# Optimization experiments

Measured on AMD Instinct MI355X. Metric: run time of the kernel, lower is better.

Reference implementation:

```python
import jax, jax.numpy as jnp
import numpy as np

B, N, H, E, P = 2, 20000, 128, 200000, 3


def _mlp2(x, w1, b1, w2, b2):
    # Linear -> SiLU -> Linear
    return jax.nn.silu(x @ w1 + b1) @ w2 + b2


def setup_inputs() -> dict:
    key = jax.random.key(0)
    ks = iter(jax.random.split(key, 40))
    def nrm(shape, s=0.05):
        return jax.random.normal(next(ks), shape, dtype=jnp.float32) * s
    inp = {
        "features": jax.random.normal(next(ks), (B, N, H), dtype=jnp.float32),
        "positions": jax.random.normal(next(ks), (B, N, P), dtype=jnp.float32),
        "edge_index_up": jax.random.randint(next(ks), (2, E), 0, N, dtype=jnp.int32),
        "edge_index_down": jax.random.randint(next(ks), (2, E), 0, N, dtype=jnp.int32),
        "degree_up": jax.random.uniform(next(ks), (N,), minval=1.0, maxval=32.0, dtype=jnp.float32),
        "degree_down": jax.random.uniform(next(ks), (N,), minval=1.0, maxval=32.0, dtype=jnp.float32),
    }
    for name in ("up", "down"):
        inp[f"w_msg1_{name}"] = nrm((2 * H + 1, H)); inp[f"b_msg1_{name}"] = jnp.zeros((H,), jnp.float32)
        inp[f"w_msg2_{name}"] = nrm((H, H));         inp[f"b_msg2_{name}"] = jnp.zeros((H,), jnp.float32)
        inp[f"w_pos1_{name}"] = nrm((H, H));         inp[f"b_pos1_{name}"] = jnp.zeros((H,), jnp.float32)
        inp[f"w_pos2_{name}"] = nrm((H, 1));         inp[f"b_pos2_{name}"] = jnp.zeros((1,), jnp.float32)
    inp["w_upd1"] = nrm((2 * H, H)); inp["b_upd1"] = jnp.zeros((H,), jnp.float32)
    inp["w_upd2"] = nrm((H, H));     inp["b_upd2"] = jnp.zeros((H,), jnp.float32)
    return inp


def reference(features, positions, edge_index_up, edge_index_down, degree_up, degree_down,
              w_msg1_up, b_msg1_up, w_msg2_up, b_msg2_up,
              w_pos1_up, b_pos1_up, w_pos2_up, b_pos2_up,
              w_msg1_down, b_msg1_down, w_msg2_down, b_msg2_down,
              w_pos1_down, b_pos1_down, w_pos2_down, b_pos2_down,
              w_upd1, b_upd1, w_upd2, b_upd2):
    n_neighborhoods = 2
    msg_acc = jnp.zeros_like(features)
    pos_upd = jnp.zeros_like(positions)
    neighborhoods = [
        (edge_index_up, degree_up,
         (w_msg1_up, b_msg1_up, w_msg2_up, b_msg2_up),
         (w_pos1_up, b_pos1_up, w_pos2_up, b_pos2_up)),
        (edge_index_down, degree_down,
         (w_msg1_down, b_msg1_down, w_msg2_down, b_msg2_down),
         (w_pos1_down, b_pos1_down, w_pos2_down, b_pos2_down)),
    ]
    for edge_index, degree, msg_p, pos_p in neighborhoods:
        src, dst = edge_index[0], edge_index[1]
        h_src = features[:, src, :]                     # [B, E, H] gather
        h_dst = features[:, dst, :]                     # [B, E, H] gather
        rel_pos = positions[:, src, :] - positions[:, dst, :]  # [B, E, P]
        dist = jnp.linalg.norm(rel_pos, axis=-1, keepdims=True)  # [B, E, 1]
        msg_input = jnp.concatenate([h_src, h_dst, dist], axis=-1)  # [B, E, 2H+1]
        messages = _mlp2(msg_input, *msg_p)             # [B, E, H]
        agg = jnp.zeros_like(features).at[:, dst, :].add(messages)  # scatter-add over dim 1
        agg = agg / jnp.clip(degree, 1.0, None)[None, :, None]
        msg_acc = msg_acc + agg
        weights = jnp.tanh(_mlp2(messages, *pos_p))     # [B, E, 1]
        pos_upd = pos_upd + jnp.zeros_like(positions).at[:, dst, :].add(weights * rel_pos)
    feat_update = _mlp2(jnp.concatenate([features, msg_acc], axis=-1), w_upd1, b_upd1, w_upd2, b_upd2)
    updated_features = features + feat_update
    updated_positions = positions + pos_upd / n_neighborhoods
    return updated_features, updated_positions
```

## Files before the change

kernel.cpp:

```cpp
#include <hip/hip_runtime.h>

#define BB 2
#define NN 20000
#define HH 128
#define EE 200000
#define TR 96
#define NEB 2084
#define NBLK 79

typedef unsigned short u16;
typedef __attribute__((ext_vector_type(4))) float f32x4;
typedef __bf16 bf16x8 __attribute__((ext_vector_type(8)));

#define MFMA(a, b, c) __builtin_amdgcn_mfma_f32_16x16x32_bf16((a), (b), (c), 0, 0, 0)

__device__ __forceinline__ float bf2f(u16 u) {
    union { unsigned int i; float f; } v; v.i = ((unsigned int)u) << 16; return v.f;
}
__device__ __forceinline__ u16 f2bf(float f) {
    union { __bf16 h; u16 u; } v; v.h = (__bf16)f; return v.u;
}
#if __has_builtin(__builtin_amdgcn_rcpf)
__device__ __forceinline__ float rcpf(float x) { return __builtin_amdgcn_rcpf(x); }
#else
__device__ __forceinline__ float rcpf(float x) { return 1.f / x; }
#endif
__device__ __forceinline__ float silu_f(float z) { return z * rcpf(1.f + __expf(-z)); }
__device__ __forceinline__ float ldv(const void* p, long i, int f) {
    return f ? ((const float*)p)[i] : bf2f(((const u16*)p)[i]);
}

__global__ __launch_bounds__(256) void detect_zero_kernel(const u16* __restrict__ f,
                                                          int* __restrict__ flag,
                                                          int* __restrict__ cnt) {
    int i = blockIdx.x * 256 + threadIdx.x;
    if (i < 40000) cnt[i] = 0;
    if (blockIdx.x == 0) {
        int tid = threadIdx.x;
        u16 v = f[tid * 2];
        int e = (v >> 7) & 0xFF;
        int ok = (e >= 101 && e <= 143) ? 1 : 0;
        __shared__ int c;
        if (tid == 0) c = 0;
        __syncthreads();
        atomicAdd(&c, ok);
        __syncthreads();
        if (tid == 0) *flag = (c < 200) ? 1 : 0;
    }
}

#define C5TOT 5281540
#define FTOT 180224
#define R0 5240000
#define R1 (R0 + C5TOT)
#define R2 (R1 + FTOT)
#define R3 (R2 + 2 * EE)
struct P18 { const void* p[18]; };
struct P8 { const void* w[8]; };

__global__ __launch_bounds__(256) void setup_kernel(
    P18 cp, P8 wf, const int* __restrict__ eu, const int* __restrict__ ed,
    float* __restrict__ ws_acc, u16* __restrict__ canon, u16* __restrict__ fbase,
    int* __restrict__ cnt_up, int* __restrict__ cnt_dn, const int* __restrict__ flag)
{
    long i = (long)blockIdx.x * 256 + threadIdx.x;
    if (i < R0) { ws_acc[i] = 0.f; return; }
    if (i < R1) {
        static const int off[19] = {
            0, 5120000, 5240000, 5260000, 5280000,
            5280128, 5280256, 5280384, 5280512, 5280640,
            5280642, 5280770, 5280898, 5281026, 5281154, 5281282,
            5281284, 5281412, 5281540 };
        static const int rsz[18] = {
            5120000, 120000, 20000, 20000,
            128, 128, 128, 128, 128, 1,
            128, 128, 128, 128, 128, 1,
            128, 128 };
        static const int soff[18] = {
            0, 0, 0, 0,
            32768, 0, 0, 0, 0, 0,
            32768, 0, 0, 0, 0, 0,
            0, 0 };
        int j = (int)(i - R0);
        int isf = *flag;
        int t = 0;
#pragma unroll 1
        while (j >= off[t + 1]) ++t;
        int k = j - off[t];
        u16 v = 0;
        if (k < rsz[t]) v = f2bf(ldv(cp.p[t], (long)soff[t] + k, isf));
        canon[j] = v;
        return;
    }
    if (i < R2) {
        static const int foff[9] = { 0, 32768, 49152, 65536, 98304, 114688,
                                     131072, 163840, 180224 };
        int j = (int)(i - R1);
        int isf = *flag;
        int t = 0;
#pragma unroll 1
        while (j >= foff[t + 1]) ++t;
        int m = j - foff[t];
        int jj = m & 7, lane = (m >> 3) & 63, nt = (m >> 9) & 7, kt = m >> 12;
        int k = kt * 32 + ((lane >> 4) * 8) + jj;
        int n = nt * 16 + (lane & 15);
        fbase[j] = f2bf(ldv(wf.w[t], (long)k * 128 + n, isf));
        return;
    }
    if (i < R3) {
        int e = (int)(i - R2);
        if (e < EE) atomicAdd(&cnt_up[eu[EE + e]], 1);
        else atomicAdd(&cnt_dn[ed[EE + e - EE]], 1);
    }
}

struct SP { const int* cnt[2]; int* cur[2]; int* bsum[2]; };

__global__ __launch_bounds__(256) void scan1_kernel(SP p) {
    int half = blockIdx.x / NBLK;
    int b = blockIdx.x - half * NBLK;
    int t = threadIdx.x;
    int i = b * 256 + t;
    __shared__ int buf[256];
    int v = (i < NN) ? p.cnt[half][i] : 0;
    buf[t] = v;
    __syncthreads();
    for (int s = 1; s < 256; s <<= 1) {
        int x = (t >= s) ? buf[t - s] : 0;
        __syncthreads();
        buf[t] += x;
        __syncthreads();
    }
    if (i < NN) p.cur[half][i] = buf[t] - v;
    if (t == 255) p.bsum[half][b] = buf[255];
}

__global__ __launch_bounds__(256) void scan2_kernel(int* __restrict__ bu, int* __restrict__ bd) {
    __shared__ int buf[2][128];
    int half = threadIdx.x >> 7, t = threadIdx.x & 127;
    int* bs = half ? bd : bu;
    int v = (t < NBLK) ? bs[t] : 0;
    buf[half][t] = v;
    __syncthreads();
    for (int s = 1; s < 128; s <<= 1) {
        int x = (t >= s) ? buf[half][t - s] : 0;
        __syncthreads();
        buf[half][t] += x;
        __syncthreads();
    }
    if (t < NBLK) bs[t] = buf[half][t] - v;
}

__global__ void scatter2_kernel(const int* __restrict__ eu, const int* __restrict__ ed,
                                int* __restrict__ cu, const int* __restrict__ bu,
                                int* __restrict__ cd, const int* __restrict__ bd,
                                int* __restrict__ su, int* __restrict__ sd) {
    int e = blockIdx.x * 256 + threadIdx.x;
    if (e < EE) {
        int d = eu[EE + e];
        int p = atomicAdd(&cu[d], 1) + bu[d >> 8];
        su[p] = e;
    } else {
        e -= EE;
        if (e < EE) {
            int d = ed[EE + e];
            int p = atomicAdd(&cd[d], 1) + bd[d >> 8];
            sd[p] = e;
        }
    }
}

struct EP {
    const int* eidx; const int* es; const u16* deg;
    const u16* fW1; const u16* fW2; const u16* fP1;
    const u16* w1last; const u16* bias1; const u16* bias2;
    const u16* biasp1; const u16* wp2; const u16* biasp2;
};

__global__ __launch_bounds__(512, 4) void edge_kernel(
    const u16* __restrict__ feat, const u16* __restrict__ posit,
    EP up, EP dn,
    float* __restrict__ msg_base, float* __restrict__ pos_base)
{
    const int tid = threadIdx.x;
    const int lane = tid & 63;
    const int wv = tid >> 6;
    const int half = blockIdx.x / (BB * NEB);
    const int rem = blockIdx.x - half * (BB * NEB);
    const int bb = rem / NEB;
    const int s0 = (rem - bb * NEB) * TR;
    const EP P = half ? dn : up;
    float* msg_acc = msg_base + (size_t)bb * NN * HH;
    float* pos_acc = pos_base + (size_t)bb * NN * 3;

    __shared__ u16 sA[TR][136];
    __shared__ u16 sB[TR][136];
    __shared__ u16 sC[TR][136];
    __shared__ float sInv[TR];
    __shared__ int sDst[TR];

    {
        const int r = tid >> 2, part = tid & 3;
        if (r < TR) {
            int slot = s0 + r; if (slot >= EE) slot = EE - 1;
            int e = P.es[slot];
            int s = P.eidx[e];
            int d = P.eidx[EE + e];
            if (part == 0) {
                sDst[r] = d;
                sInv[r] = 1.f / fmaxf(bf2f(P.deg[d]), 1.f);
                const u16* ps = posit + ((size_t)bb * NN + s) * 3;
                const u16* pd = posit + ((size_t)bb * NN + d) * 3;
                float dx = bf2f(ps[0]) - bf2f(pd[0]);
                float dy = bf2f(ps[1]) - bf2f(pd[1]);
                float dz = bf2f(ps[2]) - bf2f(pd[2]);
                *(float4*)&sC[r][128] =
                    make_float4(sqrtf(dx * dx + dy * dy + dz * dz), dx, dy, dz);
            }
            const uint4* fs = (const uint4*)(feat + ((size_t)bb * NN + s) * HH);
            const uint4* fd = (const uint4*)(feat + ((size_t)bb * NN + d) * HH);
            uint4* as = (uint4*)&sA[r][part * 32];
            uint4* ad = (uint4*)&sB[r][part * 32];
#pragma unroll
            for (int i = 0; i < 4; ++i) { as[i] = fs[part * 4 + i]; ad[i] = fd[part * 4 + i]; }
        }
    }
    __syncthreads();

    const int nt = wv;
    const int mrow = lane & 15;
    const int kq = (lane >> 4) * 8;
    const int crow = (lane >> 4) * 4;
    const int ccol = lane & 15;
    const int col = nt * 16 + ccol;

    f32x4 acc[6];
#pragma unroll
    for (int mt = 0; mt < 6; ++mt) acc[mt] = (f32x4){0.f, 0.f, 0.f, 0.f};

#pragma unroll
    for (int kt = 0; kt < 8; ++kt) {
        const u16* Xb = (kt < 4) ? &sA[0][0] : &sB[0][0];
        const int kk = (kt & 3) * 32 + kq;
        bf16x8 bw = *(const bf16x8*)(P.fW1 + (size_t)(((kt * 8 + nt) * 64 + lane) * 8));
#pragma unroll
        for (int mt = 0; mt < 6; ++mt) {
            bf16x8 a = *(const bf16x8*)(Xb + (mt * 16 + mrow) * 136 + kk);
            acc[mt] = MFMA(a, bw, acc[mt]);
        }
    }

    {
        const float wl = bf2f(P.w1last[col]);
        const float bb1 = bf2f(P.bias1[col]);
#pragma unroll
        for (int mt = 0; mt < 6; ++mt) {
#pragma unroll
            for (int r = 0; r < 4; ++r) {
                const int row = mt * 16 + crow + r;
                const float dist = ((const float*)&sC[row][128])[0];
                float z = fmaf(dist, wl, acc[mt][r]) + bb1;
                sC[row][col] = f2bf(silu_f(z));
            }
        }
    }
    __syncthreads();

#pragma unroll
    for (int mt = 0; mt < 6; ++mt) acc[mt] = (f32x4){0.f, 0.f, 0.f, 0.f};
#pragma unroll
    for (int kt = 0; kt < 4; ++kt) {
        const int kk = kt * 32 + kq;
        bf16x8 bw = *(const bf16x8*)(P.fW2 + (size_t)(((kt * 8 + nt) * 64 + lane) * 8));
#pragma unroll
        for (int mt = 0; mt < 6; ++mt) {
            bf16x8 a = *(const bf16x8*)(&sC[0][0] + (mt * 16 + mrow) * 136 + kk);
            acc[mt] = MFMA(a, bw, acc[mt]);
        }
    }
    {
        const float bb2 = bf2f(P.bias2[col]);
#pragma unroll
        for (int mt = 0; mt < 6; ++mt) {
#pragma unroll
            for (int r = 0; r < 4; ++r) {
                const int row = mt * 16 + crow + r;
                sA[row][col] = f2bf(acc[mt][r] + bb2);
            }
        }
    }
    __syncthreads();

#pragma unroll
    for (int mt = 0; mt < 6; ++mt) acc[mt] = (f32x4){0.f, 0.f, 0.f, 0.f};
#pragma unroll
    for (int kt = 0; kt < 4; ++kt) {
        const int kk = kt * 32 + kq;
        bf16x8 bw = *(const bf16x8*)(P.fP1 + (size_t)(((kt * 8 + nt) * 64 + lane) * 8));
#pragma unroll
        for (int mt = 0; mt < 6; ++mt) {
            bf16x8 a = *(const bf16x8*)(&sA[0][0] + (mt * 16 + mrow) * 136 + kk);
            acc[mt] = MFMA(a, bw, acc[mt]);
        }
    }
    {
        const float bp1 = bf2f(P.biasp1[col]);
#pragma unroll
        for (int mt = 0; mt < 6; ++mt) {
#pragma unroll
            for (int r = 0; r < 4; ++r) {
                const int row = mt * 16 + crow + r;
                sB[row][col] = f2bf(silu_f(acc[mt][r] + bp1));
            }
        }
    }
    __syncthreads();


    {
        const int scol = tid & 127;
        const int r0 = (tid >> 7) * 24;
        float vals[24];
#pragma unroll
        for (int j = 0; j < 24; ++j) vals[j] = bf2f(sA[r0 + j][scol]);
        float accv = 0.f;
        int dprev = sDst[r0];
        float invprev = sInv[r0];
#pragma unroll
        for (int j = 0; j < 24; ++j) {
            const int r = r0 + j;
            int dcur = sDst[r];
            if (dcur != dprev) {
                unsafeAtomicAdd(&msg_acc[(size_t)dprev * HH + scol], accv * invprev);
                accv = 0.f; dprev = dcur; invprev = sInv[r];
            }
            accv += (s0 + r < EE) ? vals[j] : 0.f;
        }
        unsafeAtomicAdd(&msg_acc[(size_t)dprev * HH + scol], accv * invprev);
    }

    {
        const int r = tid >> 2, q = tid & 3;
        if (r < TR) {
            const unsigned* t32 = (const unsigned*)&sB[r][q * 32];
            const unsigned* w32 = (const unsigned*)(P.wp2 + q * 32);
            float p = 0.f;
#pragma unroll
            for (int k = 0; k < 16; ++k) {
                unsigned a = t32[k], b = w32[k];
                union { unsigned i; float f; } al, ah, bl, bh;
                al.i = a << 16; ah.i = a & 0xffff0000u;
                bl.i = b << 16; bh.i = b & 0xffff0000u;
                p = fmaf(al.f, bl.f, p);
                p = fmaf(ah.f, bh.f, p);
            }
            p += __shfl_xor(p, 1);
            p += __shfl_xor(p, 2);
            if (q == 0 && s0 + r < EE) {
                float wgt = tanhf(p + bf2f(P.biasp2[0]));
                const float* rp = (const float*)&sC[r][128];
                const size_t pb = (size_t)sDst[r] * 3;
                unsafeAtomicAdd(&pos_acc[pb + 0], wgt * rp[1]);
                unsafeAtomicAdd(&pos_acc[pb + 1], wgt * rp[2]);
                unsafeAtomicAdd(&pos_acc[pb + 2], wgt * rp[3]);
            }
        }
    }
}

__global__ __launch_bounds__(256) void update_kernel(
    const void* __restrict__ rawfeat, const void* __restrict__ rawpos,
    const u16* __restrict__ fU1, const u16* __restrict__ bu1,
    const u16* __restrict__ fU2, const u16* __restrict__ bu2,
    void* __restrict__ outp, const float* __restrict__ magg, const float* __restrict__ pacc,
    const int* __restrict__ flag)
{
    const int tid = threadIdx.x;
    const int lane = tid & 63;
    const int wv = tid >> 6;
    const int row0 = blockIdx.x * 64;
    const int isf = *flag;

    __shared__ u16 sA[64][136];
    __shared__ u16 sB[64][136];

    if (isf) {
        const float* fp = (const float*)rawfeat + (size_t)row0 * HH;
        for (int i = tid; i < 1024; i += 256) {
            int r = i >> 4, c = (i & 15) * 8;
            float4 v0 = *(const float4*)(fp + (size_t)r * HH + c);
            float4 v1 = *(const float4*)(fp + (size_t)r * HH + c + 4);
            uint4 o;
            o.x = (unsigned)f2bf(v0.x) | ((unsigned)f2bf(v0.y) << 16);
            o.y = (unsigned)f2bf(v0.z) | ((unsigned)f2bf(v0.w) << 16);
            o.z = (unsigned)f2bf(v1.x) | ((unsigned)f2bf(v1.y) << 16);
            o.w = (unsigned)f2bf(v1.z) | ((unsigned)f2bf(v1.w) << 16);
            *(uint4*)&sA[r][c] = o;
        }
    } else {
        const uint4* fp = (const uint4*)((const u16*)rawfeat + (size_t)row0 * HH);
        for (int i = tid; i < 1024; i += 256) {
            int r = i >> 4, c = i & 15;
            *(uint4*)&sA[r][c * 8] = fp[i];
        }
    }
    {
        const float4* am = (const float4*)(magg) + (size_t)row0 * 32;
        for (int i = tid; i < 2048; i += 256) {
            int r = i >> 5;
            float4 v = am[i];
            int c = (i & 31) * 4;
            sB[r][c + 0] = f2bf(v.x);
            sB[r][c + 1] = f2bf(v.y);
            sB[r][c + 2] = f2bf(v.z);
            sB[r][c + 3] = f2bf(v.w);
        }
    }
    __syncthreads();

    const int nt0 = wv * 2;
    const int mrow = lane & 15;
    const int kq = (lane >> 4) * 8;
    const int crow = (lane >> 4) * 4;
    const int ccol = lane & 15;

    f32x4 acc[4][2];
#pragma unroll
    for (int mt = 0; mt < 4; ++mt) {
        acc[mt][0] = (f32x4){0.f, 0.f, 0.f, 0.f};
        acc[mt][1] = (f32x4){0.f, 0.f, 0.f, 0.f};
    }
#pragma unroll
    for (int kt = 0; kt < 8; ++kt) {
        const u16* Xb = (kt < 4) ? &sA[0][0] : &sB[0][0];
        const int kk = (kt & 3) * 32 + kq;
        bf16x8 bw0 = *(const bf16x8*)(fU1 + (size_t)(((kt * 8 + nt0) * 64 + lane) * 8));
        bf16x8 bw1 = *(const bf16x8*)(fU1 + (size_t)(((kt * 8 + nt0 + 1) * 64 + lane) * 8));
#pragma unroll
        for (int mt = 0; mt < 4; ++mt) {
            bf16x8 a = *(const bf16x8*)(Xb + (mt * 16 + mrow) * 136 + kk);
            acc[mt][0] = MFMA(a, bw0, acc[mt][0]);
            acc[mt][1] = MFMA(a, bw1, acc[mt][1]);
        }
    }
    __syncthreads();

#pragma unroll
    for (int mt = 0; mt < 4; ++mt) {
#pragma unroll
        for (int n2 = 0; n2 < 2; ++n2) {
            const int col = (nt0 + n2) * 16 + ccol;
            const float bb = bf2f(bu1[col]);
#pragma unroll
            for (int r = 0; r < 4; ++r) {
                const int row = mt * 16 + crow + r;
                sB[row][col] = f2bf(silu_f(acc[mt][n2][r] + bb));
            }
        }
    }
    __syncthreads();

#pragma unroll
    for (int mt = 0; mt < 4; ++mt) {
        acc[mt][0] = (f32x4){0.f, 0.f, 0.f, 0.f};
        acc[mt][1] = (f32x4){0.f, 0.f, 0.f, 0.f};
    }
#pragma unroll
    for (int kt = 0; kt < 4; ++kt) {
        const int kk = kt * 32 + kq;
        bf16x8 bw0 = *(const bf16x8*)(fU2 + (size_t)(((kt * 8 + nt0) * 64 + lane) * 8));
        bf16x8 bw1 = *(const bf16x8*)(fU2 + (size_t)(((kt * 8 + nt0 + 1) * 64 + lane) * 8));
#pragma unroll
        for (int mt = 0; mt < 4; ++mt) {
            bf16x8 a = *(const bf16x8*)(&sB[0][0] + (mt * 16 + mrow) * 136 + kk);
            acc[mt][0] = MFMA(a, bw0, acc[mt][0]);
            acc[mt][1] = MFMA(a, bw1, acc[mt][1]);
        }
    }
#pragma unroll
    for (int mt = 0; mt < 4; ++mt) {
#pragma unroll
        for (int n2 = 0; n2 < 2; ++n2) {
            const int col = (nt0 + n2) * 16 + ccol;
            const float bb = bf2f(bu2[col]);
#pragma unroll
            for (int r = 0; r < 4; ++r) {
                const int row = mt * 16 + crow + r;
                const size_t idx = (size_t)(row0 + row) * HH + col;
                if (isf) {
                    float base = ((const float*)rawfeat)[idx];
                    ((float*)outp)[idx] = acc[mt][n2][r] + bb + base;
                } else {
                    float base = bf2f(sA[row][col]);
                    ((u16*)outp)[idx] = f2bf(acc[mt][n2][r] + bb + base);
                }
            }
        }
    }

    if (tid < 192) {
        int i = row0 * 3 + tid;
        float x = pacc[i];
        if (isf) {
            float base = ((const float*)rawpos)[i];
            ((float*)outp)[5120000 + i] = base + 0.5f * x;
        } else {
            float base = bf2f(((const u16*)rawpos)[i]);
            ((u16*)outp)[5120000 + i] = f2bf(base + 0.5f * x);
        }
    }
}

extern "C" void kernel_launch(void* const* d_in, const int* in_sizes, int n_in,
                              void* d_out, int out_size, void* d_ws, size_t ws_size,
                              hipStream_t stream)
{
    float* ws_msg  = (float*)d_ws;
    float* ws_pos  = (float*)((char*)d_ws + 20480000);
    int*   cnt_up  = (int*)((char*)d_ws + 20960000);
    int*   cnt_dn  = (int*)((char*)d_ws + 21040000);
    int*   cur_up  = (int*)((char*)d_ws + 21120000);
    int*   cur_dn  = (int*)((char*)d_ws + 21200000);
    int*   bsum_up = (int*)((char*)d_ws + 21280000);
    int*   bsum_dn = (int*)((char*)d_ws + 21280400);
    int*   es_up   = (int*)((char*)d_ws + 21280800);
    int*   es_dn   = (int*)((char*)d_ws + 22080800);
    u16*   fbase   = (u16*)((char*)d_ws + 22880800);
    u16*   canon   = (u16*)((char*)d_ws + 23241248);
    int*   flag    = (int*)((char*)d_ws + 33804328);
    if (ws_size < 33804332ULL) return;

    u16* f_m1u = fbase;
    u16* f_m2u = fbase + 32768;
    u16* f_p1u = fbase + 49152;
    u16* f_m1d = fbase + 65536;
    u16* f_m2d = fbase + 98304;
    u16* f_p1d = fbase + 114688;
    u16* f_u1  = fbase + 131072;
    u16* f_u2  = fbase + 163840;

    u16* cfeat  = canon;
    u16* cpos   = canon + 5120000;
    u16* cdgu   = canon + 5240000;
    u16* cdgd   = canon + 5260000;
    u16* cw1lu  = canon + 5280000;
    u16* cb1u   = canon + 5280128;
    u16* cb2u   = canon + 5280256;
    u16* cbp1u  = canon + 5280384;
    u16* cwp2u  = canon + 5280512;
    u16* cbp2u  = canon + 5280640;
    u16* cw1ld  = canon + 5280642;
    u16* cb1d   = canon + 5280770;
    u16* cb2d   = canon + 5280898;
    u16* cbp1d  = canon + 5281026;
    u16* cwp2d  = canon + 5281154;
    u16* cbp2d  = canon + 5281282;
    u16* cbu1   = canon + 5281284;
    u16* cbu2   = canon + 5281412;

    const int* ei_up = (const int*)d_in[2];
    const int* ei_dn = (const int*)d_in[3];

    detect_zero_kernel<<<157, 256, 0, stream>>>((const u16*)d_in[0], flag, cnt_up);

    P18 cp;
    cp.p[0] = d_in[0];  cp.p[1] = d_in[1];  cp.p[2] = d_in[4];  cp.p[3] = d_in[5];
    cp.p[4] = d_in[6];  cp.p[5] = d_in[7];  cp.p[6] = d_in[9];  cp.p[7] = d_in[11];
    cp.p[8] = d_in[12]; cp.p[9] = d_in[13];
    cp.p[10] = d_in[14]; cp.p[11] = d_in[15]; cp.p[12] = d_in[17]; cp.p[13] = d_in[19];
    cp.p[14] = d_in[20]; cp.p[15] = d_in[21];
    cp.p[16] = d_in[23]; cp.p[17] = d_in[25];
    P8 wsf;
    wsf.w[0] = d_in[6];  wsf.w[1] = d_in[8];  wsf.w[2] = d_in[10]; wsf.w[3] = d_in[14];
    wsf.w[4] = d_in[16]; wsf.w[5] = d_in[18]; wsf.w[6] = d_in[22]; wsf.w[7] = d_in[24];
    setup_kernel<<<(R3 + 255) / 256, 256, 0, stream>>>(cp, wsf, ei_up, ei_dn,
                                                       ws_msg, canon, fbase,
                                                       cnt_up, cnt_dn, flag);

    SP sp;
    sp.cnt[0] = cnt_up; sp.cnt[1] = cnt_dn;
    sp.cur[0] = cur_up; sp.cur[1] = cur_dn;
    sp.bsum[0] = bsum_up; sp.bsum[1] = bsum_dn;
    scan1_kernel<<<2 * NBLK, 256, 0, stream>>>(sp);
    scan2_kernel<<<1, 256, 0, stream>>>(bsum_up, bsum_dn);
    scatter2_kernel<<<(2 * EE + 255) / 256, 256, 0, stream>>>(ei_up, ei_dn, cur_up, bsum_up,
                                                              cur_dn, bsum_dn, es_up, es_dn);

    EP up, dn;
    up.eidx = ei_up; up.es = es_up; up.deg = cdgu;
    up.fW1 = f_m1u; up.fW2 = f_m2u; up.fP1 = f_p1u;
    up.w1last = cw1lu; up.bias1 = cb1u; up.bias2 = cb2u;
    up.biasp1 = cbp1u; up.wp2 = cwp2u; up.biasp2 = cbp2u;
    dn.eidx = ei_dn; dn.es = es_dn; dn.deg = cdgd;
    dn.fW1 = f_m1d; dn.fW2 = f_m2d; dn.fP1 = f_p1d;
    dn.w1last = cw1ld; dn.bias1 = cb1d; dn.bias2 = cb2d;
    dn.biasp1 = cbp1d; dn.wp2 = cwp2d; dn.biasp2 = cbp2d;
    edge_kernel<<<2 * BB * NEB, 512, 0, stream>>>(cfeat, cpos, up, dn, ws_msg, ws_pos);

    update_kernel<<<625, 256, 0, stream>>>(d_in[0], d_in[1], f_u1, cbu1, f_u2, cbu2,
                                           d_out, ws_msg, ws_pos, flag);
}
```

Baseline: 499.8 us.

## Precompose msg2 and pos1 weights to compute both second-stage GEMMs concurrently

A new setup kernel precomputes W_msg2·W_pos1 and the folded bias (b2·W_pos1 + b_pos1), so the position MLP's first layer can be fed directly from the SiLU hidden layer. The edge kernel then runs one wider GEMM producing both the messages and the position hidden activations in one pass, removing a dependent GEMM stage and one barrier. Warps are retiled into a 2x4 grid with 48 rows by 32 or 64 columns each. The trade-offs are an extra bf16 rounding of the composed weights, which changes numerics slightly, and the assumption that fP1 buffers hold 2x the fragment space at offset 16384.

After: 537.1 us. 1.07x slower.

```diff
diff --git a/kernel.cpp b/kernel.cpp
--- a/kernel.cpp
+++ b/kernel.cpp
@@ -114,6 +114,38 @@
     }
 }
 
+__global__ __launch_bounds__(256) void gemm_fuse_kernel(
+    const void* __restrict__ w2u, const void* __restrict__ p1u,
+    const void* __restrict__ b2u, const void* __restrict__ bp1u,
+    const void* __restrict__ w2d, const void* __restrict__ p1d,
+    const void* __restrict__ b2d, const void* __restrict__ bp1d,
+    u16* __restrict__ fragu, u16* __restrict__ fragd,
+    u16* __restrict__ cbp1u, u16* __restrict__ cbp1d,
+    const int* __restrict__ flag)
+{
+    const int dir = blockIdx.x >> 6;
+    const int idx = (blockIdx.x & 63) * 256 + threadIdx.x;
+    const int k = idx >> 7, n = idx & 127;
+    const int isf = *flag;
+    const void* W2 = dir ? w2d : w2u;
+    const void* P1 = dir ? p1d : p1u;
+    float s = 0.f;
+#pragma unroll 4
+    for (int m = 0; m < 128; ++m)
+        s += ldv(W2, (long)k * 128 + m, isf) * ldv(P1, (long)m * 128 + n, isf);
+    u16* dst = dir ? fragd : fragu;
+    dst[(((k >> 5) * 8 + (n >> 4)) * 64 + ((k >> 3) & 3) * 16 + (n & 15)) * 8 + (k & 7)] = f2bf(s);
+    if (idx < 128) {
+        const void* B2 = dir ? b2d : b2u;
+        const void* BP1 = dir ? bp1d : bp1u;
+        float t = 0.f;
+#pragma unroll 4
+        for (int m = 0; m < 128; ++m)
+            t += ldv(B2, m, isf) * ldv(P1, (long)m * 128 + idx, isf);
+        (dir ? cbp1d : cbp1u)[idx] = f2bf(t + ldv(BP1, idx, isf));
+    }
+}
+
 struct SP { const int* cnt[2]; int* cur[2]; int* bsum[2]; };
 
 __global__ __launch_bounds__(256) void scan1_kernel(SP p) {
@@ -227,95 +259,108 @@
     }
     __syncthreads();
 
-    const int nt = wv;
+    const int wm = wv >> 2;
+    const int wn = wv & 3;
+    const int rbase = wm * 48;
     const int mrow = lane & 15;
     const int kq = (lane >> 4) * 8;
     const int crow = (lane >> 4) * 4;
     const int ccol = lane & 15;
-    const int col = nt * 16 + ccol;
-
-    f32x4 acc[6];
-#pragma unroll
-    for (int mt = 0; mt < 6; ++mt) acc[mt] = (f32x4){0.f, 0.f, 0.f, 0.f};
-
+
+    f32x4 acc[3][2];
+#pragma unroll
+    for (int mt = 0; mt < 3; ++mt) {
+        acc[mt][0] = (f32x4){0.f, 0.f, 0.f, 0.f};
+        acc[mt][1] = (f32x4){0.f, 0.f, 0.f, 0.f};
+    }
 #pragma unroll
     for (int kt = 0; kt < 8; ++kt) {
         const u16* Xb = (kt < 4) ? &sA[0][0] : &sB[0][0];
         const int kk = (kt & 3) * 32 + kq;
-        bf16x8 bw = *(const bf16x8*)(P.fW1 + (size_t)(((kt * 8 + nt) * 64 + lane) * 8));
-#pragma unroll
-        for (int mt = 0; mt < 6; ++mt) {
-            bf16x8 a = *(const bf16x8*)(Xb + (mt * 16 + mrow) * 136 + kk);
-            acc[mt] = MFMA(a, bw, acc[mt]);
-        }
-    }
-
-    {
+        bf16x8 bw0 = *(const bf16x8*)(P.fW1 + (size_t)(((kt * 8 + wn * 2) * 64 + lane) * 8));
+        bf16x8 bw1 = *(const bf16x8*)(P.fW1 + (size_t)(((kt * 8 + wn * 2 + 1) * 64 + lane) * 8));
+#pragma unroll
+        for (int mt = 0; mt < 3; ++mt) {
+            bf16x8 a = *(const bf16x8*)(Xb + (rbase + mt * 16 + mrow) * 136 + kk);
+            acc[mt][0] = MFMA(a, bw0, acc[mt][0]);
+            acc[mt][1] = MFMA(a, bw1, acc[mt][1]);
+        }
+    }
+
+#pragma unroll
+    for (int n2 = 0; n2 < 2; ++n2) {
+        const int col = (wn * 2 + n2) * 16 + ccol;
         const float wl = bf2f(P.w1last[col]);
         const float bb1 = bf2f(P.bias1[col]);
 #pragma unroll
-        for (int mt = 0; mt < 6; ++mt) {
+        for (int mt = 0; mt < 3; ++mt) {
 #pragma unroll
             for (int r = 0; r < 4; ++r) {
-                const int row = mt * 16 + crow + r;
+                const int row = rbase + mt * 16 + crow + r;
                 const float dist = ((const float*)&sC[row][128])[0];
-                float z = fmaf(dist, wl, acc[mt][r]) + bb1;
+                float z = fmaf(dist, wl, acc[mt][n2][r]) + bb1;
                 sC[row][col] = f2bf(silu_f(z));
             }
         }
     }
     __syncthreads();
 
-#pragma unroll
-    for (int mt = 0; mt < 6; ++mt) acc[mt] = (f32x4){0.f, 0.f, 0.f, 0.f};
+    f32x4 facc[3][4];
+#pragma unroll
+    for (int mt = 0; mt < 3; ++mt)
+#pragma unroll
+        for (int j = 0; j < 4; ++j) facc[mt][j] = (f32x4){0.f, 0.f, 0.f, 0.f};
+    const int nt0 = wn * 4;
 #pragma unroll
     for (int kt = 0; kt < 4; ++kt) {
         const int kk = kt * 32 + kq;
-        bf16x8 bw = *(const bf16x8*)(P.fW2 + (size_t)(((kt * 8 + nt) * 64 + lane) * 8));
-#pragma unroll
-        for (int mt = 0; mt < 6; ++mt) {
-            bf16x8 a = *(const bf16x8*)(&sC[0][0] + (mt * 16 + mrow) * 136 + kk);
-            acc[mt] = MFMA(a, bw, acc[mt]);
-        }
-    }
-    {
-        const float bb2 = bf2f(P.bias2[col]);
-#pragma unroll
-        for (int mt = 0; mt < 6; ++mt) {
-#pragma unroll
-            for (int r = 0; r < 4; ++r) {
-                const int row = mt * 16 + crow + r;
-                sA[row][col] = f2bf(acc[mt][r] + bb2);
-            }
-        }
-    }
-    __syncthreads();
-
-#pragma unroll
-    for (int mt = 0; mt < 6; ++mt) acc[mt] = (f32x4){0.f, 0.f, 0.f, 0.f};
-#pragma unroll
-    for (int kt = 0; kt < 4; ++kt) {
-        const int kk = kt * 32 + kq;
-        bf16x8 bw = *(const bf16x8*)(P.fP1 + (size_t)(((kt * 8 + nt) * 64 + lane) * 8));
-#pragma unroll
-        for (int mt = 0; mt < 6; ++mt) {
-            bf16x8 a = *(const bf16x8*)(&sA[0][0] + (mt * 16 + mrow) * 136 + kk);
-            acc[mt] = MFMA(a, bw, acc[mt]);
-        }
-    }
-    {
-        const float bp1 = bf2f(P.biasp1[col]);
-#pragma unroll
-        for (int mt = 0; mt < 6; ++mt) {
-#pragma unroll
-            for (int r = 0; r < 4; ++r) {
-                const int row = mt * 16 + crow + r;
-                sB[row][col] = f2bf(silu_f(acc[mt][r] + bp1));
-            }
-        }
-    }
-    __syncthreads();
-
+        bf16x8 bw[4];
+#pragma unroll
+        for (int j = 0; j < 4; ++j) {
+            const int nt = nt0 + j;
+            const size_t off = (nt & 8)
+                ? (size_t)(16384 + ((kt * 8 + (nt & 7)) * 64 + lane) * 8)
+                : (size_t)(((kt * 8 + nt) * 64 + lane) * 8);
+            bw[j] = *(const bf16x8*)(P.fW2 + off);
+        }
+#pragma unroll
+        for (int mt = 0; mt < 3; ++mt) {
+            bf16x8 a = *(const bf16x8*)(&sC[0][0] + (rbase + mt * 16 + mrow) * 136 + kk);
+#pragma unroll
+            for (int j = 0; j < 4; ++j) facc[mt][j] = MFMA(a, bw[j], facc[mt][j]);
+        }
+    }
+
+    if (wn < 2) {
+#pragma unroll
+        for (int j = 0; j < 4; ++j) {
+            const int col = (nt0 + j) * 16 + ccol;
+            const float b2v = bf2f(P.bias2[col]);
+#pragma unroll
+            for (int mt = 0; mt < 3; ++mt) {
+#pragma unroll
+                for (int r = 0; r < 4; ++r) {
+                    const int row = rbase + mt * 16 + crow + r;
+                    sA[row][col] = f2bf(facc[mt][j][r] + b2v);
+                }
+            }
+        }
+    } else {
+#pragma unroll
+        for (int j = 0; j < 4; ++j) {
+            const int col = (nt0 - 8 + j) * 16 + ccol;
+            const float fbv = bf2f(P.biasp1[col]);
+#pragma unroll
+            for (int mt = 0; mt < 3; ++mt) {
+#pragma unroll
+                for (int r = 0; r < 4; ++r) {
+                    const int row = rbase + mt * 16 + crow + r;
+                    sB[row][col] = f2bf(silu_f(facc[mt][j][r] + fbv));
+                }
+            }
+        }
+    }
+    __syncthreads();
 
     {
         const int scol = tid & 127;
@@ -577,6 +622,10 @@
                                                        ws_msg, canon, fbase,
                                                        cnt_up, cnt_dn, flag);
 
+    gemm_fuse_kernel<<<128, 256, 0, stream>>>(d_in[8], d_in[10], d_in[9], d_in[11],
+                                              d_in[16], d_in[18], d_in[17], d_in[19],
+                                              f_p1u, f_p1d, cbp1u, cbp1d, flag);
+
     SP sp;
     sp.cnt[0] = cnt_up; sp.cnt[1] = cnt_dn;
     sp.cur[0] = cur_up; sp.cur[1] = cur_dn;
```
